# Optimization experiments

Measured on AMD Instinct MI355X. Metric: run time of the kernel, lower is better.

## Reference

```python
import jax, jax.numpy as jnp
import numpy as np

B, T, D_IN, D, H, FF, K, L = 4, 1024, 560, 512, 4, 2048, 11, 6
DK = D // H
PAD = (K - 1) // 2  # sanm_shfit=0 -> left=5, right=5
EPS = 1e-5
CLAMP = 60000.0


def setup_inputs() -> dict:
    key = jax.random.key(0)
    ks = jax.random.split(key, 16)
    s = 0.02
    return {
        "x": jax.random.normal(ks[0], (B, T, D_IN), jnp.float32),
        "mask": jnp.ones((B, 1, T), jnp.float32),
        # layer 0 (in_size=D_IN -> size=D, no attn residual)
        "ln1_w0": jnp.ones((D_IN,), jnp.float32), "ln1_b0": jnp.zeros((D_IN,), jnp.float32),
        "qkv_w0": jax.random.normal(ks[1], (D_IN, 3 * D), jnp.float32) * s,
        "qkv_b0": jnp.zeros((3 * D,), jnp.float32),
        "out_w0": jax.random.normal(ks[2], (D, D), jnp.float32) * s,
        "out_b0": jnp.zeros((D,), jnp.float32),
        "fsmn_w0": jax.random.normal(ks[3], (D, K), jnp.float32) * s,
        "ln2_w0": jnp.ones((D,), jnp.float32), "ln2_b0": jnp.zeros((D,), jnp.float32),
        "ffn_w1_0": jax.random.normal(ks[4], (D, FF), jnp.float32) * s,
        "ffn_b1_0": jnp.zeros((FF,), jnp.float32),
        "ffn_w2_0": jax.random.normal(ks[5], (FF, D), jnp.float32) * s,
        "ffn_b2_0": jnp.zeros((D,), jnp.float32),
        # layers 1..L-1 stacked
        "ln1_w": jnp.ones((L - 1, D), jnp.float32), "ln1_b": jnp.zeros((L - 1, D), jnp.float32),
        "qkv_w": jax.random.normal(ks[6], (L - 1, D, 3 * D), jnp.float32) * s,
        "qkv_b": jnp.zeros((L - 1, 3 * D), jnp.float32),
        "out_w": jax.random.normal(ks[7], (L - 1, D, D), jnp.float32) * s,
        "out_b": jnp.zeros((L - 1, D), jnp.float32),
        "fsmn_w": jax.random.normal(ks[8], (L - 1, D, K), jnp.float32) * s,
        "ln2_w": jnp.ones((L - 1, D), jnp.float32), "ln2_b": jnp.zeros((L - 1, D), jnp.float32),
        "ffn_w1": jax.random.normal(ks[9], (L - 1, D, FF), jnp.float32) * s,
        "ffn_b1": jnp.zeros((L - 1, FF), jnp.float32),
        "ffn_w2": jax.random.normal(ks[10], (L - 1, FF, D), jnp.float32) * s,
        "ffn_b2": jnp.zeros((L - 1, D), jnp.float32),
        "after_ln_w": jnp.ones((D,), jnp.float32), "after_ln_b": jnp.zeros((D,), jnp.float32),
    }


def layer_norm(x, g, b):
    m = x.mean(-1, keepdims=True)
    v = ((x - m) ** 2).mean(-1, keepdims=True)
    return (x - m) * jax.lax.rsqrt(v + EPS) * g + b


def dw_conv(x, w):
    # x: (B,T,D); depthwise conv along time, asymmetric const pad (PAD, K-1-PAD)
    xc = jnp.transpose(x, (0, 2, 1))  # (B,D,T)
    xc = jnp.pad(xc, ((0, 0), (0, 0), (PAD, K - 1 - PAD)))
    y = jax.lax.conv_general_dilated(
        xc, w[:, None, :], (1,), 'VALID',
        dimension_numbers=('NCH', 'OIH', 'NCH'), feature_group_count=D)
    return jnp.transpose(y, (0, 2, 1))  # (B,T,D)


def sanm_attn(xn, mask, qkv_w, qkv_b, out_w, out_b, fsmn_w):
    b, t, _ = xn.shape
    qkv = xn @ qkv_w + qkv_b
    q, k, v = jnp.split(qkv, 3, axis=-1)  # each (B,T,D)
    # FSMN memory branch on v
    m3 = jnp.reshape(mask, (b, -1, 1))  # (B,T,1)
    vm = v * m3
    mem = (dw_conv(vm, fsmn_w) + vm) * m3
    # multi-head attention
    qh = q.reshape(b, t, H, DK).transpose(0, 2, 1, 3) * (DK ** -0.5)
    kh = k.reshape(b, t, H, DK).transpose(0, 2, 1, 3)
    vh = v.reshape(b, t, H, DK).transpose(0, 2, 1, 3)
    scores = jnp.einsum('bhqd,bhkd->bhqk', qh, kh)
    m4 = (mask[:, None, :, :] == 0.0)  # (B,1,1,T)
    scores = jnp.where(m4, -jnp.inf, scores)
    attn = jnp.where(m4, 0.0, jax.nn.softmax(scores, axis=-1))
    ctx = jnp.einsum('bhqk,bhkd->bhqd', attn, vh)
    ctx = ctx.transpose(0, 2, 1, 3).reshape(b, t, D)
    return ctx @ out_w + out_b + mem


def encoder_layer(x, mask, p, residual_attn):
    (ln1_w, ln1_b, qkv_w, qkv_b, out_w, out_b, fsmn_w,
     ln2_w, ln2_b, w1, b1, w2, b2) = p
    res = x
    xn = layer_norm(x, ln1_w, ln1_b)
    a = sanm_attn(xn, mask, qkv_w, qkv_b, out_w, out_b, fsmn_w)
    x = res + a if residual_attn else a
    res = x
    xn = layer_norm(x, ln2_w, ln2_b)
    x = res + (jax.nn.relu(xn @ w1 + b1) @ w2 + b2)
    return jnp.clip(x, -CLAMP, CLAMP)


def pos_encode(t, depth):
    half = depth // 2
    log_inc = jnp.log(jnp.float32(10000.0)) / (half - 1)
    inv = jnp.exp(jnp.arange(half, dtype=jnp.float32) * -log_inc)
    pos = jnp.arange(1, t + 1, dtype=jnp.float32)
    st = pos[None, :, None] * inv[None, None, :]
    return jnp.concatenate([jnp.sin(st), jnp.cos(st)], axis=-1)  # (1,T,depth)


def reference(x, mask,
              ln1_w0, ln1_b0, qkv_w0, qkv_b0, out_w0, out_b0, fsmn_w0,
              ln2_w0, ln2_b0, ffn_w1_0, ffn_b1_0, ffn_w2_0, ffn_b2_0,
              ln1_w, ln1_b, qkv_w, qkv_b, out_w, out_b, fsmn_w,
              ln2_w, ln2_b, ffn_w1, ffn_b1, ffn_w2, ffn_b2,
              after_ln_w, after_ln_b):
    x = x * (D ** 0.5) + pos_encode(T, D_IN)
    p0 = (ln1_w0, ln1_b0, qkv_w0, qkv_b0, out_w0, out_b0, fsmn_w0,
          ln2_w0, ln2_b0, ffn_w1_0, ffn_b1_0, ffn_w2_0, ffn_b2_0)
    x = encoder_layer(x, mask, p0, residual_attn=False)
    for i in range(L - 1):
        p = (ln1_w[i], ln1_b[i], qkv_w[i], qkv_b[i], out_w[i], out_b[i], fsmn_w[i],
             ln2_w[i], ln2_b[i], ffn_w1[i], ffn_b1[i], ffn_w2[i], ffn_b2[i])
        x = encoder_layer(x, mask, p, residual_attn=True)
    return layer_norm(x, after_ln_w, after_ln_b)
```

## Files before the change

### kernel.cpp

```cpp
#include <hip/hip_runtime.h>
#include <cmath>

#define Bb 4
#define Tt 1024
#define DIN 560
#define Dd 512
#define FFd 2048
#define Ll 6
#define BT (Bb * Tt)
#define QKV_N (3 * Dd)

typedef unsigned short u16;
typedef unsigned int u32;
typedef __attribute__((ext_vector_type(8))) short short8;
typedef __attribute__((ext_vector_type(4))) float f32x4;

static __device__ __forceinline__ u16 f2bf(float f) {
    u32 u = __float_as_uint(f);
    return (u16)((u + 0x7fffu + ((u >> 16) & 1u)) >> 16);
}
static __device__ __forceinline__ float bf2f(u16 h) { return __uint_as_float((u32)h << 16); }

static __device__ __forceinline__ f32x4 MFMA(short8 a, short8 b, f32x4 c) {
    return __builtin_amdgcn_mfma_f32_16x16x32_bf16(a, b, c, 0, 0, 0);
}

static __device__ __forceinline__ void gload16(const u16* g, u16* l) {
    __builtin_amdgcn_global_load_lds(
        (const __attribute__((address_space(1))) void*)g,
        (__attribute__((address_space(3))) void*)l, 16, 0, 0);
}

__global__ __launch_bounds__(256) void prep_kernel(const float* __restrict__ x,
                                                   float* __restrict__ out) {
    int idx = blockIdx.x * 256 + threadIdx.x;
    int d = idx % DIN;
    int bt = idx / DIN;
    int t = bt & (Tt - 1);
    const float log_inc = 9.210340371976184f / 279.0f;
    int i = (d < 280) ? d : d - 280;
    float ang = (float)(t + 1) * expf(-(float)i * log_inc);
    float pe = (d < 280) ? sinf(ang) : cosf(ang);
    out[idx] = x[idx] * 22.627416997969522f + pe;
}

__global__ __launch_bounds__(256) void ln_kernel(const float* __restrict__ in,
                                                 float* __restrict__ out,
                                                 const float* __restrict__ g,
                                                 const float* __restrict__ be, int W) {
    __shared__ float red[8];
    const int row = blockIdx.x;
    const float* xr = in + (size_t)row * W;
    float s = 0.f, s2 = 0.f;
    for (int i = threadIdx.x; i < W; i += 256) { float v = xr[i]; s += v; s2 += v * v; }
    for (int off = 32; off; off >>= 1) { s += __shfl_xor(s, off); s2 += __shfl_xor(s2, off); }
    int w = threadIdx.x >> 6;
    if ((threadIdx.x & 63) == 0) { red[w] = s; red[4 + w] = s2; }
    __syncthreads();
    s = red[0] + red[1] + red[2] + red[3];
    s2 = red[4] + red[5] + red[6] + red[7];
    float mean = s / W;
    float var = s2 / W - mean * mean;
    float rs = rsqrtf(var + 1e-5f);
    float* yr = out + (size_t)row * W;
    for (int i = threadIdx.x; i < W; i += 256)
        yr[i] = (xr[i] - mean) * rs * g[i] + be[i];
}

__global__ __launch_bounds__(256) void ln_split_kernel(const float* __restrict__ in, int Win,
                                                       u16* __restrict__ out, int Wp,
                                                       const float* __restrict__ g,
                                                       const float* __restrict__ be) {
    __shared__ float red[8];
    const int row = blockIdx.x;
    const float* xr = in + (size_t)row * Win;
    float s = 0.f, s2 = 0.f;
    for (int i = threadIdx.x; i < Win; i += 256) { float v = xr[i]; s += v; s2 += v * v; }
    for (int off = 32; off; off >>= 1) { s += __shfl_xor(s, off); s2 += __shfl_xor(s2, off); }
    int w = threadIdx.x >> 6;
    if ((threadIdx.x & 63) == 0) { red[w] = s; red[4 + w] = s2; }
    __syncthreads();
    s = red[0] + red[1] + red[2] + red[3];
    s2 = red[4] + red[5] + red[6] + red[7];
    float mean = s / Win;
    float var = s2 / Win - mean * mean;
    float rs = rsqrtf(var + 1e-5f);
    u16* yr = out + (size_t)row * 3 * Wp;
    for (int i = threadIdx.x; i < (Wp >> 2); i += 256) {
        int k = i << 2;
        u16 u[12];
#pragma unroll
        for (int j = 0; j < 4; ++j) {
            float v = (k + j < Win) ? (xr[k + j] - mean) * rs * g[k + j] + be[k + j] : 0.f;
            u16 hi = f2bf(v); float rem = v - bf2f(hi); u16 lo = f2bf(rem);
            u[j * 3] = hi; u[j * 3 + 1] = lo; u[j * 3 + 2] = hi;
        }
        uint2* dst = (uint2*)(yr + 3 * k);
        dst[0] = {(u32)u[0] | ((u32)u[1] << 16), (u32)u[2] | ((u32)u[3] << 16)};
        dst[1] = {(u32)u[4] | ((u32)u[5] << 16), (u32)u[6] | ((u32)u[7] << 16)};
        dst[2] = {(u32)u[8] | ((u32)u[9] << 16), (u32)u[10] | ((u32)u[11] << 16)};
    }
}

__global__ __launch_bounds__(256) void cvtw_kernel(const float* __restrict__ W,
                                                   u16* __restrict__ out,
                                                   int K, int Kp, int N) {
    __shared__ float tile[32][33];
    int k0 = blockIdx.x * 32, n0 = blockIdx.y * 32;
    int tid = threadIdx.x;
    int col = tid & 31, r0 = tid >> 5;
#pragma unroll
    for (int p = 0; p < 4; ++p) {
        int k = k0 + r0 + p * 8;
        tile[r0 + p * 8][col] = (k < K) ? W[(size_t)k * N + n0 + col] : 0.f;
    }
    __syncthreads();
    int n = tid >> 3, kc = (tid & 7) << 2;
    u16 u[12];
#pragma unroll
    for (int i = 0; i < 4; ++i) {
        float v = tile[kc + i][n];
        u16 hi = f2bf(v); float rem = v - bf2f(hi); u16 lo = f2bf(rem);
        u[i * 3] = hi; u[i * 3 + 1] = hi; u[i * 3 + 2] = lo;
    }
    u16* dst = out + (size_t)(n0 + n) * 3 * Kp + 3 * (k0 + kc);
    uint2* q = (uint2*)dst;
    q[0] = {(u32)u[0] | ((u32)u[1] << 16), (u32)u[2] | ((u32)u[3] << 16)};
    q[1] = {(u32)u[4] | ((u32)u[5] << 16), (u32)u[6] | ((u32)u[7] << 16)};
    q[2] = {(u32)u[8] | ((u32)u[9] << 16), (u32)u[10] | ((u32)u[11] << 16)};
}

template<int TM, int TN, int MODE>
__global__ __launch_bounds__(256) void gemm_bf16(
    const u16* __restrict__ A, int lda,
    const u16* __restrict__ Bw, int ldb,
    const float* __restrict__ bias,
    const float* __restrict__ add1,
    const float* __restrict__ add2,
    void* __restrict__ Cout, int N, int Kd, int do_clamp)
{
    constexpr int ISS_A = TM * 8 / 256;
    constexpr int ISS_B = TN * 8 / 256;
    constexpr int WM = TM / 2, WN = TN / 2;
    constexpr int FM = WM / 16, FN = WN / 16;
    __shared__ u16 As[TM * 64];
    __shared__ u16 Bs[TN * 64];
    const int tid = threadIdx.x;
    const int lane = tid & 63, wid = tid >> 6;
    const int wm = wid >> 1, wn = wid & 1;
    const int lr = lane & 15, lg = lane >> 4;
    const int m0 = blockIdx.y * TM, n0 = blockIdx.x * TN;
    const f32x4 fzero = {0.f, 0.f, 0.f, 0.f};
    f32x4 acc[FM][FN];
#pragma unroll
    for (int i = 0; i < FM; ++i)
#pragma unroll
        for (int j = 0; j < FN; ++j) acc[i][j] = fzero;

    const int nk = Kd >> 6;
    for (int kt = 0; kt < nk; ++kt) {
        const int k0 = kt << 6;
#pragma unroll
        for (int i = 0; i < ISS_A; ++i) {
            int slot = i * 256 + tid;
            int row = slot >> 3, c = slot & 7;
            gload16(A + (size_t)(m0 + row) * lda + k0 + ((c ^ (row & 7)) << 3), &As[slot << 3]);
        }
#pragma unroll
        for (int i = 0; i < ISS_B; ++i) {
            int slot = i * 256 + tid;
            int row = slot >> 3, c = slot & 7;
            gload16(Bw + (size_t)(n0 + row) * ldb + k0 + ((c ^ (row & 7)) << 3), &Bs[slot << 3]);
        }
        __syncthreads();
#pragma unroll
        for (int ks = 0; ks < 2; ++ks) {
            short8 av[FM], bv[FN];
#pragma unroll
            for (int mf = 0; mf < FM; ++mf) {
                int row = wm * WM + mf * 16 + lr;
                int c = ks * 4 + lg;
                av[mf] = *(const short8*)&As[((row << 3) + (c ^ (row & 7))) << 3];
            }
#pragma unroll
            for (int nf = 0; nf < FN; ++nf) {
                int row = wn * WN + nf * 16 + lr;
                int c = ks * 4 + lg;
                bv[nf] = *(const short8*)&Bs[((row << 3) + (c ^ (row & 7))) << 3];
            }
#pragma unroll
            for (int mf = 0; mf < FM; ++mf)
#pragma unroll
                for (int nf = 0; nf < FN; ++nf)
                    acc[mf][nf] = MFMA(av[mf], bv[nf], acc[mf][nf]);
        }
        __syncthreads();
    }
#pragma unroll
    for (int mf = 0; mf < FM; ++mf)
#pragma unroll
        for (int nf = 0; nf < FN; ++nf)
#pragma unroll
            for (int r = 0; r < 4; ++r) {
                int grow = m0 + wm * WM + mf * 16 + lg * 4 + r;
                int gcol = n0 + wn * WN + nf * 16 + lr;
                float v = acc[mf][nf][r] + bias[gcol];
                if constexpr (MODE == 0) {
                    size_t off = (size_t)grow * N + gcol;
                    if (add1) v += add1[off];
                    if (add2) v += add2[off];
                    if (do_clamp) v = fminf(fmaxf(v, -60000.f), 60000.f);
                    ((float*)Cout)[off] = v;
                } else if constexpr (MODE == 1) {
                    ((u16*)Cout)[(size_t)grow * N + gcol] = f2bf(v);
                } else {
                    v = fmaxf(v, 0.f);
                    u16 hi = f2bf(v); float rem = v - bf2f(hi); u16 lo = f2bf(rem);
                    u16* p = (u16*)Cout + (size_t)grow * 3 * N + 3 * gcol;
                    p[0] = hi; p[1] = lo; p[2] = hi;
                }
            }
}

__global__ __launch_bounds__(256) void fsmn_kernel(const u16* __restrict__ qkv,
                                                   const float* __restrict__ mask,
                                                   const float* __restrict__ w,
                                                   float* __restrict__ mem) {
    int g = blockIdx.x * 256 + threadIdx.x;
    int bt = g >> 6;
    int d0 = (g & 63) << 3;
    int t = bt & (Tt - 1), b = bt >> 10;
    float acc[8] = {0.f, 0.f, 0.f, 0.f, 0.f, 0.f, 0.f, 0.f};
#pragma unroll
    for (int j = 0; j < 11; ++j) {
        int tt = t + j - 5;
        if (tt < 0 || tt >= Tt) continue;
        float mk = mask[b * Tt + tt];
        union { uint4 q; u16 s[8]; } U;
        U.q = *(const uint4*)(qkv + (size_t)(b * Tt + tt) * QKV_N + 1024 + d0);
#pragma unroll
        for (int e = 0; e < 8; ++e)
            acc[e] += bf2f(U.s[e]) * mk * w[(d0 + e) * 11 + j];
    }
    float mk0 = mask[b * Tt + t];
    union { uint4 q; u16 s[8]; } U0;
    U0.q = *(const uint4*)(qkv + (size_t)bt * QKV_N + 1024 + d0);
    float out[8];
#pragma unroll
    for (int e = 0; e < 8; ++e) {
        float vm = bf2f(U0.s[e]) * mk0;
        out[e] = (acc[e] + vm) * mk0;
    }
    float4 o0 = {out[0], out[1], out[2], out[3]};
    float4 o1 = {out[4], out[5], out[6], out[7]};
    float* mp = mem + (size_t)bt * Dd + d0;
    *(float4*)mp = o0; *(float4*)(mp + 4) = o1;
}

__global__ __launch_bounds__(256) void vtrans_kernel(const u16* __restrict__ qkv,
                                                     u16* __restrict__ vt) {
    __shared__ u16 tile[32][33];
    int bh = blockIdx.z, b = bh >> 2, h = bh & 3;
    int t0 = blockIdx.x * 32, d0 = blockIdx.y * 32;
    int tid = threadIdx.x;
    int col = tid & 31, r0 = tid >> 5;
#pragma unroll
    for (int p = 0; p < 4; ++p) {
        int tl = r0 + p * 8;
        tile[tl][col] = qkv[(size_t)(b * Tt + t0 + tl) * QKV_N + 1024 + h * 128 + d0 + col];
    }
    __syncthreads();
    int dl = tid >> 3, tc = (tid & 7) << 2;
    u16 u[4];
#pragma unroll
    for (int i = 0; i < 4; ++i) u[i] = tile[tc + i][dl];
    uint2 val = {(u32)u[0] | ((u32)u[1] << 16), (u32)u[2] | ((u32)u[3] << 16)};
    *(uint2*)(vt + (size_t)(bh * 128 + d0 + dl) * Tt + t0 + tc) = val;
}

__global__ __launch_bounds__(256) void attn_kernel(const u16* __restrict__ qkv,
                                                   const u16* __restrict__ vt,
                                                   const float* __restrict__ mask,
                                                   u16* __restrict__ ctx3) {
    __shared__ u16 Qs[64 * 128];
    __shared__ u16 Ks[64 * 128];
    __shared__ u16 Vs[128 * 64];
    __shared__ u16 Ps[4][16 * 72];
    __shared__ float mLds[Tt];
    const int tid = threadIdx.x;
    const int lane = tid & 63, wid = tid >> 6;
    const int lr = lane & 15, lg = lane >> 4;
    int L = blockIdx.x;
    int xcd = L & 7, slot = L >> 3;
    int bh = (slot >= 16) ? xcd + 8 : xcd;
    int qt = slot & 15;
    int b = bh >> 2, h = bh & 3;
    const size_t base = (size_t)b * Tt * QKV_N;
    const int q0 = qt * 64;
    const float c2 = 0.08838834764831845f * 1.44269504088896340736f;

#pragma unroll
    for (int i = 0; i < 4; ++i) {
        int s = i * 256 + tid;
        int row = s >> 4, c = s & 15;
        gload16(qkv + base + (size_t)(q0 + row) * QKV_N + h * 128 + ((c ^ (row & 7)) << 3),
                &Qs[s << 3]);
    }
    for (int i = tid; i < Tt; i += 256) mLds[i] = mask[b * Tt + i];

    const f32x4 fzero = {0.f, 0.f, 0.f, 0.f};
    f32x4 o[8];
#pragma unroll
    for (int i = 0; i < 8; ++i) o[i] = fzero;
    float mrun[4] = {-3e38f, -3e38f, -3e38f, -3e38f};
    float lrun[4] = {0.f, 0.f, 0.f, 0.f};

    for (int kvt = 0; kvt < 16; ++kvt) {
        int t0 = kvt * 64;
#pragma unroll
        for (int i = 0; i < 4; ++i) {
            int s = i * 256 + tid;
            int row = s >> 4, c = s & 15;
            gload16(qkv + base + (size_t)(t0 + row) * QKV_N + 512 + h * 128 + ((c ^ (row & 7)) << 3),
                    &Ks[s << 3]);
        }
#pragma unroll
        for (int i = 0; i < 4; ++i) {
            int s = i * 256 + tid;
            int row = s >> 3, c = s & 7;
            gload16(vt + (size_t)(bh * 128 + row) * Tt + t0 + ((c ^ (row & 7)) << 3),
                    &Vs[s << 3]);
        }
        __syncthreads();

        f32x4 s4[4] = {fzero, fzero, fzero, fzero};
#pragma unroll
        for (int ks = 0; ks < 4; ++ks) {
            int qrow = wid * 16 + lr;
            int c = ks * 4 + lg;
            short8 aq = *(const short8*)&Qs[((qrow << 4) + (c ^ (qrow & 7))) << 3];
#pragma unroll
            for (int nf = 0; nf < 4; ++nf) {
                int krow = nf * 16 + lr;
                short8 bk = *(const short8*)&Ks[((krow << 4) + (c ^ (krow & 7))) << 3];
                s4[nf] = MFMA(aq, bk, s4[nf]);
            }
        }
        float tmax[4] = {-3e38f, -3e38f, -3e38f, -3e38f};
#pragma unroll
        for (int nf = 0; nf < 4; ++nf) {
            float mv = mLds[t0 + nf * 16 + lr];
#pragma unroll
            for (int r = 0; r < 4; ++r) {
                float sv = s4[nf][r] + ((mv == 0.f) ? -1e30f : 0.f);
                s4[nf][r] = sv;
                tmax[r] = fmaxf(tmax[r], sv);
            }
        }
#pragma unroll
        for (int off = 8; off >= 1; off >>= 1)
#pragma unroll
            for (int r = 0; r < 4; ++r) tmax[r] = fmaxf(tmax[r], __shfl_xor(tmax[r], off));
        float rs[4];
#pragma unroll
        for (int r = 0; r < 4; ++r) {
            float mnew = fmaxf(mrun[r], tmax[r]);
            float ex = exp2f((mrun[r] - mnew) * c2);
            mrun[r] = mnew; lrun[r] *= ex; rs[r] = ex;
        }
#pragma unroll
        for (int nf = 0; nf < 8; ++nf)
#pragma unroll
            for (int r = 0; r < 4; ++r) o[nf][r] *= rs[r];
        float psum[4] = {0.f, 0.f, 0.f, 0.f};
#pragma unroll
        for (int nf = 0; nf < 4; ++nf)
#pragma unroll
            for (int r = 0; r < 4; ++r) {
                float pv = exp2f((s4[nf][r] - mrun[r]) * c2);
                psum[r] += pv;
                Ps[wid][(lg * 4 + r) * 72 + nf * 16 + lr] = f2bf(pv);
            }
#pragma unroll
        for (int off = 8; off >= 1; off >>= 1)
#pragma unroll
            for (int r = 0; r < 4; ++r) psum[r] += __shfl_xor(psum[r], off);
#pragma unroll
        for (int r = 0; r < 4; ++r) lrun[r] += psum[r];

#pragma unroll
        for (int ks2 = 0; ks2 < 2; ++ks2) {
            short8 pa = *(const short8*)&Ps[wid][lr * 72 + ks2 * 32 + lg * 8];
#pragma unroll
            for (int nf = 0; nf < 8; ++nf) {
                int vrow = nf * 16 + lr;
                int c = ks2 * 4 + lg;
                short8 vb = *(const short8*)&Vs[((vrow << 3) + (c ^ (vrow & 7))) << 3];
                o[nf] = MFMA(pa, vb, o[nf]);
            }
        }
        __syncthreads();
    }
    float inv[4];
#pragma unroll
    for (int r = 0; r < 4; ++r) inv[r] = 1.f / lrun[r];
#pragma unroll
    for (int nf = 0; nf < 8; ++nf)
#pragma unroll
        for (int r = 0; r < 4; ++r) {
            int grow = b * Tt + q0 + wid * 16 + lg * 4 + r;
            int gcol = h * 128 + nf * 16 + lr;
            float v = o[nf][r] * inv[r];
            u16 hi = f2bf(v); float rem = v - bf2f(hi); u16 lo = f2bf(rem);
            u16* p = ctx3 + (size_t)grow * 1536 + 3 * gcol;
            p[0] = hi; p[1] = lo; p[2] = hi;
        }
}

extern "C" void kernel_launch(void* const* d_in, const int* in_sizes, int n_in,
                              void* d_out, int out_size, void* d_ws, size_t ws_size,
                              hipStream_t stream) {
    const float* x    = (const float*)d_in[0];
    const float* mask = (const float*)d_in[1];

    char* p = (char*)d_ws;
    float* X   = (float*)p; p += 9175040;
    float* X2  = (float*)p; p += 8388608;
    u16*   XN3 = (u16*)p;   p += 14155776;
    u16*   QKVb= (u16*)p;   p += 12582912;
    float* MEM = (float*)p; p += 8388608;
    u16*   Vt  = (u16*)p;   p += 4194304;
    u16*   W3  = (u16*)p;   p += 6291456;
    u16*   FFH3 = QKVb;
    u16*   CTX3 = XN3;

    prep_kernel<<<(BT * DIN) / 256, 256, 0, stream>>>(x, X);

    for (int l = 0; l < Ll; ++l) {
        const float *ln1w, *ln1b, *qkvw, *qkvb, *outw, *outb, *fsmnw;
        const float *ln2w, *ln2b, *w1, *b1, *w2, *b2;
        if (l == 0) {
            ln1w = (const float*)d_in[2];  ln1b = (const float*)d_in[3];
            qkvw = (const float*)d_in[4];  qkvb = (const float*)d_in[5];
            outw = (const float*)d_in[6];  outb = (const float*)d_in[7];
            fsmnw = (const float*)d_in[8];
            ln2w = (const float*)d_in[9];  ln2b = (const float*)d_in[10];
            w1 = (const float*)d_in[11];   b1 = (const float*)d_in[12];
            w2 = (const float*)d_in[13];   b2 = (const float*)d_in[14];
        } else {
            int i = l - 1;
            ln1w = (const float*)d_in[15] + (size_t)i * Dd;
            ln1b = (const float*)d_in[16] + (size_t)i * Dd;
            qkvw = (const float*)d_in[17] + (size_t)i * Dd * QKV_N;
            qkvb = (const float*)d_in[18] + (size_t)i * QKV_N;
            outw = (const float*)d_in[19] + (size_t)i * Dd * Dd;
            outb = (const float*)d_in[20] + (size_t)i * Dd;
            fsmnw = (const float*)d_in[21] + (size_t)i * Dd * 11;
            ln2w = (const float*)d_in[22] + (size_t)i * Dd;
            ln2b = (const float*)d_in[23] + (size_t)i * Dd;
            w1 = (const float*)d_in[24] + (size_t)i * Dd * FFd;
            b1 = (const float*)d_in[25] + (size_t)i * FFd;
            w2 = (const float*)d_in[26] + (size_t)i * FFd * Dd;
            b2 = (const float*)d_in[27] + (size_t)i * Dd;
        }
        const int Win = (l == 0) ? DIN : Dd;
        const int Kp  = (l == 0) ? 576 : 512;
        const int ld3 = 3 * Kp;

        cvtw_kernel<<<dim3(Kp / 32, QKV_N / 32), 256, 0, stream>>>(qkvw, W3, Win, Kp, QKV_N);
        ln_split_kernel<<<BT, 256, 0, stream>>>(X, Win, XN3, Kp, ln1w, ln1b);
        gemm_bf16<128, 128, 1><<<dim3(QKV_N / 128, BT / 128), 256, 0, stream>>>(
            XN3, ld3, W3, ld3, qkvb, nullptr, nullptr, QKVb, QKV_N, ld3, 0);
        cvtw_kernel<<<dim3(16, 16), 256, 0, stream>>>(outw, W3, Dd, Dd, Dd);
        fsmn_kernel<<<(BT * 64) / 256, 256, 0, stream>>>(QKVb, mask, fsmnw, MEM);
        vtrans_kernel<<<dim3(32, 4, 16), 256, 0, stream>>>(QKVb, Vt);
        attn_kernel<<<256, 256, 0, stream>>>(QKVb, Vt, mask, CTX3);
        gemm_bf16<128, 64, 0><<<dim3(Dd / 64, BT / 128), 256, 0, stream>>>(
            CTX3, 1536, W3, 1536, outb, MEM, (l == 0) ? nullptr : X, X2, Dd, 1536, 0);
        ln_split_kernel<<<BT, 256, 0, stream>>>(X2, Dd, XN3, Dd, ln2w, ln2b);
        for (int hh = 0; hh < 2; ++hh) {
            size_t ro = (size_t)hh * 2048;
            cvtw_kernel<<<dim3(16, 64), 256, 0, stream>>>(w1, W3, Dd, Dd, FFd);
            gemm_bf16<128, 128, 2><<<dim3(FFd / 128, 2048 / 128), 256, 0, stream>>>(
                XN3 + ro * 1536, 1536, W3, 1536, b1, nullptr, nullptr, FFH3, FFd, 1536, 0);
            cvtw_kernel<<<dim3(64, 16), 256, 0, stream>>>(w2, W3, FFd, FFd, Dd);
            gemm_bf16<64, 64, 0><<<dim3(Dd / 64, 2048 / 64), 256, 0, stream>>>(
                FFH3, 3 * FFd, W3, 3 * FFd, b2, X2 + ro * Dd, nullptr, X + ro * Dd,
                Dd, 3 * FFd, 1);
        }
    }

    ln_kernel<<<BT, 256, 0, stream>>>(X, (float*)d_out,
                                      (const float*)d_in[28], (const float*)d_in[29], Dd);
}
```

Before: 2.651 ms.

## Double-buffer GEMM shared tiles, shrink tiles, split FFN along hidden dim

The GEMM kernel now double-buffers its A/B shared-memory tiles, so the loads for the next K step are issued before the MFMAs on the current one. Tile heights drop from 128 to 64 rows, giving more blocks per launch for better CU occupancy. The FFN is now chunked along the 2048 hidden dimension in two 1024 halves over all 4096 rows, instead of two row halves. The second W2 GEMM accumulates into X in place and applies the clamp only there. This doubles LDS use per block and relies on in-place aliasing of add1 and the output, which is why the restrict qualifiers were removed.

Measured after the change: 2.186 ms. -17.5%, faster.

```diff
diff --git a/kernel.cpp b/kernel.cpp
--- a/kernel.cpp
+++ b/kernel.cpp
@@ -102,9 +102,9 @@
     }
 }
 
-__global__ __launch_bounds__(256) void cvtw_kernel(const float* __restrict__ W,
+__global__ __launch_bounds__(256) void cvtw_kernel(const float* __restrict__ W, int ldw,
                                                    u16* __restrict__ out,
-                                                   int K, int Kp, int N) {
+                                                   int K, int Kp) {
     __shared__ float tile[32][33];
     int k0 = blockIdx.x * 32, n0 = blockIdx.y * 32;
     int tid = threadIdx.x;
@@ -112,7 +112,7 @@
 #pragma unroll
     for (int p = 0; p < 4; ++p) {
         int k = k0 + r0 + p * 8;
-        tile[r0 + p * 8][col] = (k < K) ? W[(size_t)k * N + n0 + col] : 0.f;
+        tile[r0 + p * 8][col] = (k < K) ? W[(size_t)k * ldw + n0 + col] : 0.f;
     }
     __syncthreads();
     int n = tid >> 3, kc = (tid & 7) << 2;
@@ -135,16 +135,16 @@
     const u16* __restrict__ A, int lda,
     const u16* __restrict__ Bw, int ldb,
     const float* __restrict__ bias,
-    const float* __restrict__ add1,
-    const float* __restrict__ add2,
-    void* __restrict__ Cout, int N, int Kd, int do_clamp)
+    const float* add1,
+    const float* add2,
+    void* Cout, int N, int Kd, int do_clamp)
 {
     constexpr int ISS_A = TM * 8 / 256;
     constexpr int ISS_B = TN * 8 / 256;
     constexpr int WM = TM / 2, WN = TN / 2;
     constexpr int FM = WM / 16, FN = WN / 16;
-    __shared__ u16 As[TM * 64];
-    __shared__ u16 Bs[TN * 64];
+    __shared__ u16 As[2][TM * 64];
+    __shared__ u16 Bs[2][TN * 64];
     const int tid = threadIdx.x;
     const int lane = tid & 63, wid = tid >> 6;
     const int wm = wid >> 1, wn = wid & 1;
@@ -158,21 +158,29 @@
         for (int j = 0; j < FN; ++j) acc[i][j] = fzero;
 
     const int nk = Kd >> 6;
-    for (int kt = 0; kt < nk; ++kt) {
+    auto STAGE = [&](int buf, int kt) {
         const int k0 = kt << 6;
 #pragma unroll
         for (int i = 0; i < ISS_A; ++i) {
             int slot = i * 256 + tid;
             int row = slot >> 3, c = slot & 7;
-            gload16(A + (size_t)(m0 + row) * lda + k0 + ((c ^ (row & 7)) << 3), &As[slot << 3]);
+            gload16(A + (size_t)(m0 + row) * lda + k0 + ((c ^ (row & 7)) << 3),
+                    &As[buf][slot << 3]);
         }
 #pragma unroll
         for (int i = 0; i < ISS_B; ++i) {
             int slot = i * 256 + tid;
             int row = slot >> 3, c = slot & 7;
-            gload16(Bw + (size_t)(n0 + row) * ldb + k0 + ((c ^ (row & 7)) << 3), &Bs[slot << 3]);
-        }
-        __syncthreads();
+            gload16(Bw + (size_t)(n0 + row) * ldb + k0 + ((c ^ (row & 7)) << 3),
+                    &Bs[buf][slot << 3]);
+        }
+    };
+
+    STAGE(0, 0);
+    __syncthreads();
+    int buf = 0;
+    for (int kt = 0; kt < nk; ++kt) {
+        if (kt + 1 < nk) STAGE(buf ^ 1, kt + 1);
 #pragma unroll
         for (int ks = 0; ks < 2; ++ks) {
             short8 av[FM], bv[FN];
@@ -180,13 +188,13 @@
             for (int mf = 0; mf < FM; ++mf) {
                 int row = wm * WM + mf * 16 + lr;
                 int c = ks * 4 + lg;
-                av[mf] = *(const short8*)&As[((row << 3) + (c ^ (row & 7))) << 3];
+                av[mf] = *(const short8*)&As[buf][((row << 3) + (c ^ (row & 7))) << 3];
             }
 #pragma unroll
             for (int nf = 0; nf < FN; ++nf) {
                 int row = wn * WN + nf * 16 + lr;
                 int c = ks * 4 + lg;
-                bv[nf] = *(const short8*)&Bs[((row << 3) + (c ^ (row & 7))) << 3];
+                bv[nf] = *(const short8*)&Bs[buf][((row << 3) + (c ^ (row & 7))) << 3];
             }
 #pragma unroll
             for (int mf = 0; mf < FM; ++mf)
@@ -195,6 +203,7 @@
                     acc[mf][nf] = MFMA(av[mf], bv[nf], acc[mf][nf]);
         }
         __syncthreads();
+        buf ^= 1;
     }
 #pragma unroll
     for (int mf = 0; mf < FM; ++mf)
@@ -204,7 +213,8 @@
             for (int r = 0; r < 4; ++r) {
                 int grow = m0 + wm * WM + mf * 16 + lg * 4 + r;
                 int gcol = n0 + wn * WN + nf * 16 + lr;
-                float v = acc[mf][nf][r] + bias[gcol];
+                float v = acc[mf][nf][r];
+                if (bias) v += bias[gcol];
                 if constexpr (MODE == 0) {
                     size_t off = (size_t)grow * N + gcol;
                     if (add1) v += add1[off];
@@ -431,6 +441,7 @@
     float* MEM = (float*)p; p += 8388608;
     u16*   Vt  = (u16*)p;   p += 4194304;
     u16*   W3  = (u16*)p;   p += 6291456;
+    u16*   W3b = W3 + 1024 * 1536;
     u16*   FFH3 = QKVb;
     u16*   CTX3 = XN3;
 
@@ -467,26 +478,29 @@
         const int Kp  = (l == 0) ? 576 : 512;
         const int ld3 = 3 * Kp;
 
-        cvtw_kernel<<<dim3(Kp / 32, QKV_N / 32), 256, 0, stream>>>(qkvw, W3, Win, Kp, QKV_N);
+        cvtw_kernel<<<dim3(Kp / 32, QKV_N / 32), 256, 0, stream>>>(qkvw, QKV_N, W3, Win, Kp);
         ln_split_kernel<<<BT, 256, 0, stream>>>(X, Win, XN3, Kp, ln1w, ln1b);
-        gemm_bf16<128, 128, 1><<<dim3(QKV_N / 128, BT / 128), 256, 0, stream>>>(
+        gemm_bf16<64, 128, 1><<<dim3(QKV_N / 128, BT / 64), 256, 0, stream>>>(
             XN3, ld3, W3, ld3, qkvb, nullptr, nullptr, QKVb, QKV_N, ld3, 0);
-        cvtw_kernel<<<dim3(16, 16), 256, 0, stream>>>(outw, W3, Dd, Dd, Dd);
+        cvtw_kernel<<<dim3(16, 16), 256, 0, stream>>>(outw, Dd, W3, Dd, Dd);
         fsmn_kernel<<<(BT * 64) / 256, 256, 0, stream>>>(QKVb, mask, fsmnw, MEM);
         vtrans_kernel<<<dim3(32, 4, 16), 256, 0, stream>>>(QKVb, Vt);
         attn_kernel<<<256, 256, 0, stream>>>(QKVb, Vt, mask, CTX3);
-        gemm_bf16<128, 64, 0><<<dim3(Dd / 64, BT / 128), 256, 0, stream>>>(
+        gemm_bf16<64, 64, 0><<<dim3(Dd / 64, BT / 64), 256, 0, stream>>>(
             CTX3, 1536, W3, 1536, outb, MEM, (l == 0) ? nullptr : X, X2, Dd, 1536, 0);
         ln_split_kernel<<<BT, 256, 0, stream>>>(X2, Dd, XN3, Dd, ln2w, ln2b);
         for (int hh = 0; hh < 2; ++hh) {
-            size_t ro = (size_t)hh * 2048;
-            cvtw_kernel<<<dim3(16, 64), 256, 0, stream>>>(w1, W3, Dd, Dd, FFd);
-            gemm_bf16<128, 128, 2><<<dim3(FFd / 128, 2048 / 128), 256, 0, stream>>>(
-                XN3 + ro * 1536, 1536, W3, 1536, b1, nullptr, nullptr, FFH3, FFd, 1536, 0);
-            cvtw_kernel<<<dim3(64, 16), 256, 0, stream>>>(w2, W3, FFd, FFd, Dd);
-            gemm_bf16<64, 64, 0><<<dim3(Dd / 64, 2048 / 64), 256, 0, stream>>>(
-                FFH3, 3 * FFd, W3, 3 * FFd, b2, X2 + ro * Dd, nullptr, X + ro * Dd,
-                Dd, 3 * FFd, 1);
+            cvtw_kernel<<<dim3(16, 32), 256, 0, stream>>>(w1 + hh * 1024, FFd, W3, Dd, Dd);
+            cvtw_kernel<<<dim3(32, 16), 256, 0, stream>>>(w2 + (size_t)hh * 1024 * Dd, Dd,
+                                                          W3b, 1024, 1024);
+            gemm_bf16<64, 128, 2><<<dim3(1024 / 128, BT / 64), 256, 0, stream>>>(
+                XN3, 1536, W3, 1536, b1 + hh * 1024, nullptr, nullptr, FFH3, 1024, 1536, 0);
+            if (hh == 0)
+                gemm_bf16<64, 64, 0><<<dim3(Dd / 64, BT / 64), 256, 0, stream>>>(
+                    FFH3, 3072, W3b, 3072, b2, X2, nullptr, X, Dd, 3072, 0);
+            else
+                gemm_bf16<64, 64, 0><<<dim3(Dd / 64, BT / 64), 256, 0, stream>>>(
+                    FFH3, 3072, W3b, 3072, nullptr, X, nullptr, X, Dd, 3072, 1);
         }
     }
 
```
